# Optimization experiments

Hardware: AMD Instinct MI355X
Metric: run time of the kernel (lower is better)

The kernel has to match this reference:

```python
import jax, jax.numpy as jnp
import numpy as np

DIM = 128
NUM_HEADS = 4
WH, WW = 7, 7
N = WH * WW            # 49 tokens per window
NW = 64                # number of windows (56/7)^2
BATCH = 64
B_ = BATCH * NW        # 4096


def _relative_position_index(Wh, Ww):
    coords = np.stack(np.meshgrid(np.arange(Wh), np.arange(Ww), indexing='ij'))  # [2,Wh,Ww]
    coords = coords.reshape(2, -1)
    rel = coords[:, :, None] - coords[:, None, :]          # [2, N, N]
    rel = rel.transpose(1, 2, 0).astype(np.int64)          # [N, N, 2]
    rel[:, :, 0] += Wh - 1
    rel[:, :, 1] += Ww - 1
    rel[:, :, 0] *= 2 * Ww - 1
    return rel.sum(-1)                                     # [N, N]


def setup_inputs() -> dict:
    key = jax.random.key(0)
    ks = jax.random.split(key, 8)
    x = jax.random.normal(ks[0], (B_, N, DIM), dtype=jnp.float32)
    # Swin shift-mask: additive, 0 or large negative; random floats are fine for math check
    mask = jax.random.normal(ks[1], (NW, N, N), dtype=jnp.float32)
    qkv_w = jax.random.normal(ks[2], (DIM, 3 * DIM), dtype=jnp.float32) * 0.02
    qkv_b = jax.random.normal(ks[3], (3 * DIM,), dtype=jnp.float32) * 0.02
    proj_w = jax.random.normal(ks[4], (DIM, DIM), dtype=jnp.float32) * 0.02
    proj_b = jax.random.normal(ks[5], (DIM,), dtype=jnp.float32) * 0.02
    table_size = (2 * WH - 1) * (2 * WW - 1)  # 169
    bias_table = jax.random.normal(ks[6], (table_size, NUM_HEADS), dtype=jnp.float32) * 0.02
    rel_idx = jnp.asarray(_relative_position_index(WH, WW), dtype=jnp.int32)  # [N,N]
    return {"x": x, "mask": mask, "qkv_w": qkv_w, "qkv_b": qkv_b,
            "proj_w": proj_w, "proj_b": proj_b, "bias_table": bias_table,
            "rel_idx": rel_idx}


def reference(x, mask, qkv_w, qkv_b, proj_w, proj_b, bias_table, rel_idx):
    B, Nn, C = x.shape
    H = bias_table.shape[1]
    hd = C // H
    scale = hd ** -0.5
    # qkv projection -> [3, B, H, N, hd]
    qkv = (x @ qkv_w + qkv_b).reshape(B, Nn, 3, H, hd).transpose(2, 0, 3, 1, 4)
    q, k, v = qkv[0] * scale, qkv[1], qkv[2]
    attn = jnp.einsum('bhnd,bhmd->bhnm', q, k)  # [B,H,N,N]
    # gathered relative position bias -> [H,N,N]
    bias = bias_table[rel_idx.reshape(-1)].reshape(Nn, Nn, H).transpose(2, 0, 1)
    attn = attn + bias[None]
    nW = mask.shape[0]
    attn = attn.reshape(-1, nW, H, Nn, Nn) + mask[None, :, None].astype(attn.dtype)
    attn = jax.nn.softmax(attn.reshape(-1, H, Nn, Nn), axis=-1)
    out = jnp.einsum('bhnm,bhmd->bnhd', attn, v).reshape(B, Nn, C)
    return out @ proj_w + proj_b
```

## Files before the change

### kernel.cpp

```cpp
#include <hip/hip_runtime.h>

#define NTOK 49
#define DIMC 128
#define NH   4
#define NWIN 64
#define NBLK 4096

#define WPROJ_OFF 98304
#define BMF_OFF   131072

typedef unsigned short u16x8 __attribute__((ext_vector_type(8)));
typedef __bf16        bf16x8 __attribute__((ext_vector_type(8)));
typedef float         f32x4  __attribute__((ext_vector_type(4)));

__device__ __forceinline__ unsigned short f2bf(float f) {
  return __builtin_bit_cast(unsigned short, (__bf16)f);
}

__device__ __forceinline__ bf16x8 ld_frag(const unsigned short* p) {
  return __builtin_bit_cast(bf16x8, *(const u16x8*)p);
}

__device__ __forceinline__ bf16x8 pack_bf16x8(float4 lo, float4 hi) {
  bf16x8 r;
  r[0] = (__bf16)lo.x; r[1] = (__bf16)lo.y; r[2] = (__bf16)lo.z; r[3] = (__bf16)lo.w;
  r[4] = (__bf16)hi.x; r[5] = (__bf16)hi.y; r[6] = (__bf16)hi.z; r[7] = (__bf16)hi.w;
  return r;
}

#define MFMA(a, b, c) __builtin_amdgcn_mfma_f32_16x16x32_bf16(a, b, c, 0, 0, 0)

__global__ void prep_kernel(const float* __restrict__ qkv_w,
                            const float* __restrict__ proj_w,
                            const float* __restrict__ bias_table,
                            const int*   __restrict__ rel_idx,
                            const float* __restrict__ mask,
                            unsigned short* __restrict__ wqkv,
                            unsigned short* __restrict__ wproj,
                            float* __restrict__ bmf)
{
  const int tid = blockIdx.x * blockDim.x + threadIdx.x;
  const int nth = gridDim.x * blockDim.x;

  for (int idx = tid; idx < 4*24*64*8; idx += nth) {
    int ii = idx & 7, lane = (idx >> 3) & 63, rest = idx >> 9;
    int ct = rest % 24, kt = rest / 24;
    int k = kt*32 + ((lane >> 4) << 3) + ii;
    int c = ct*16 + (lane & 15);
    wqkv[idx] = f2bf(qkv_w[k*384 + c]);
  }
  for (int idx = tid; idx < 4*8*64*8; idx += nth) {
    int ii = idx & 7, lane = (idx >> 3) & 63, rest = idx >> 9;
    int ct = rest & 7, kt = rest >> 3;
    int k = kt*32 + ((lane >> 4) << 3) + ii;
    int c = ct*16 + (lane & 15);
    wproj[idx] = f2bf(proj_w[k*128 + c]);
  }
  for (int idx = tid; idx < NWIN*NH*16*256; idx += nth) {
    int r2   = idx & 3;
    int lane = (idx >> 2) & 63;
    int ij   = (idx >> 8) & 15;
    int h    = (idx >> 12) & 3;
    int wi   = idx >> 14;
    int i = ij >> 2, j = ij & 3;
    int r = i*16 + ((lane >> 4) << 2) + r2;
    int c = j*16 + (lane & 15);
    float v = -1e30f;
    if (r < NTOK && c < NTOK)
      v = mask[wi*2401 + r*49 + c] + bias_table[rel_idx[r*49 + c]*4 + h];
    bmf[idx] = v;
  }
}

#define SLOT 5712
__global__ __launch_bounds__(256, 3) void winattn_kernel(
    const float* __restrict__ x,
    const float* __restrict__ qkv_b,
    const float* __restrict__ proj_b,
    const unsigned short* __restrict__ wqkv,
    const unsigned short* __restrict__ wproj,
    const float* __restrict__ bmf,
    float* __restrict__ out)
{
  __shared__ __align__(16) unsigned short smem[4*SLOT];

  const int b    = blockIdx.x;
  const int wi   = b & (NWIN - 1);
  const int tid  = threadIdx.x;
  const int h    = tid >> 6;
  const int lane = tid & 63;
  const int lhi  = lane >> 4;
  const int llo  = lane & 15;

  unsigned short* slot = smem + h*SLOT;
  unsigned short* Qh  = slot;
  unsigned short* Kh  = slot + 1764;
  unsigned short* Vh  = slot + 3528;
  unsigned short* Ph  = slot;
  unsigned short* XOh = slot;

  const f32x4 zv = {0.f, 0.f, 0.f, 0.f};
  const float* xb = x + (size_t)b * (NTOK*DIMC);

  f32x4 acc[6][4];
  #pragma unroll
  for (int j = 0; j < 6; j++)
    #pragma unroll
    for (int i = 0; i < 4; i++) acc[j][i] = zv;

  #pragma unroll
  for (int kt = 0; kt < 4; kt++) {
    bf16x8 a[4];
    #pragma unroll
    for (int i = 0; i < 4; i++) {
      float4 lo = make_float4(0.f,0.f,0.f,0.f), hi = lo;
      int row = i*16 + llo;
      if (i < 3 || row < NTOK) {
        const float4* p = (const float4*)(xb + row*DIMC + kt*32 + lhi*8);
        lo = p[0]; hi = p[1];
      }
      a[i] = pack_bf16x8(lo, hi);
    }
    #pragma unroll
    for (int j = 0; j < 6; j++) {
      int ct = (j >> 1)*8 + h*2 + (j & 1);
      bf16x8 bw = ld_frag(wqkv + (((kt*24 + ct)*64 + lane) << 3));
      #pragma unroll
      for (int i = 0; i < 4; i++) acc[j][i] = MFMA(a[i], bw, acc[j][i]);
    }
  }

  float bias[6];
  #pragma unroll
  for (int j = 0; j < 6; j++)
    bias[j] = qkv_b[((j >> 1)*8 + h*2 + (j & 1))*16 + llo];

  const float scale = 0.17677669529663687f;

  #pragma unroll
  for (int j = 0; j < 2; j++) {
    int d = j*16 + llo;
    #pragma unroll
    for (int i = 0; i < 4; i++)
      #pragma unroll
      for (int r2 = 0; r2 < 4; r2++) {
        int r = i*16 + lhi*4 + r2;
        if (r < NTOK) Qh[r*36 + d] = f2bf((acc[j][i][r2] + bias[j]) * scale);
      }
  }
  #pragma unroll
  for (int j = 2; j < 4; j++) {
    int d = (j - 2)*16 + llo;
    #pragma unroll
    for (int i = 0; i < 4; i++)
      #pragma unroll
      for (int r2 = 0; r2 < 4; r2++) {
        int r = i*16 + lhi*4 + r2;
        if (r < NTOK) Kh[r*36 + d] = f2bf(acc[j][i][r2] + bias[j]);
      }
  }
  #pragma unroll
  for (int j = 4; j < 6; j++) {
    int d = (j - 4)*16 + llo;
    #pragma unroll
    for (int i = 0; i < 4; i++) {
      ushort4 pk;
      pk.x = f2bf(acc[j][i][0] + bias[j]);
      pk.y = f2bf(acc[j][i][1] + bias[j]);
      pk.z = f2bf(acc[j][i][2] + bias[j]);
      pk.w = f2bf(acc[j][i][3] + bias[j]);
      *(ushort4*)(Vh + d*68 + i*16 + lhi*4) = pk;
    }
  }

  f32x4 s[4][4];
  #pragma unroll
  for (int i = 0; i < 4; i++)
    #pragma unroll
    for (int j = 0; j < 4; j++) s[i][j] = zv;

  {
    bf16x8 qa[4];
    #pragma unroll
    for (int i = 0; i < 4; i++) qa[i] = ld_frag(Qh + (i*16 + llo)*36 + lhi*8);
    #pragma unroll
    for (int j = 0; j < 4; j++) {
      bf16x8 kb = ld_frag(Kh + (j*16 + llo)*36 + lhi*8);
      #pragma unroll
      for (int i = 0; i < 4; i++) s[i][j] = MFMA(qa[i], kb, s[i][j]);
    }
  }

  {
    const float4* bmf4 = (const float4*)bmf + (size_t)(wi*4 + h)*16*64 + lane;
    #pragma unroll
    for (int j = 0; j < 4; j++) {
      bool cok = (j*16 + llo) < NTOK;
      #pragma unroll
      for (int i = 0; i < 4; i++) {
        float4 t = bmf4[(i*4 + j)*64];
        #pragma unroll
        for (int r2 = 0; r2 < 4; r2++) {
          float v = s[i][j][r2] + (&t.x)[r2];
          s[i][j][r2] = cok ? v : -1e30f;
        }
      }
    }
  }

  #pragma unroll
  for (int i = 0; i < 4; i++) {
    #pragma unroll
    for (int r2 = 0; r2 < 4; r2++) {
      float m = fmaxf(fmaxf(s[i][0][r2], s[i][1][r2]),
                      fmaxf(s[i][2][r2], s[i][3][r2]));
      #pragma unroll
      for (int off = 1; off < 16; off <<= 1) m = fmaxf(m, __shfl_xor(m, off, 64));
      float sum = 0.f;
      #pragma unroll
      for (int j = 0; j < 4; j++) {
        float p = __expf(s[i][j][r2] - m);
        s[i][j][r2] = p;
        sum += p;
      }
      #pragma unroll
      for (int off = 1; off < 16; off <<= 1) sum += __shfl_xor(sum, off, 64);
      float inv = 1.0f / sum;
      #pragma unroll
      for (int j = 0; j < 4; j++) s[i][j][r2] *= inv;
    }
  }

  #pragma unroll
  for (int i = 0; i < 4; i++)
    #pragma unroll
    for (int r2 = 0; r2 < 4; r2++) {
      int r = i*16 + lhi*4 + r2;
      if (r < NTOK) {
        #pragma unroll
        for (int j = 0; j < 4; j++)
          Ph[r*72 + j*16 + llo] = f2bf(s[i][j][r2]);
      }
    }

  f32x4 oacc[2][4];
  #pragma unroll
  for (int nt = 0; nt < 2; nt++)
    #pragma unroll
    for (int i = 0; i < 4; i++) oacc[nt][i] = zv;

  #pragma unroll
  for (int ks = 0; ks < 2; ks++) {
    bf16x8 pa[4];
    #pragma unroll
    for (int i = 0; i < 4; i++)
      pa[i] = ld_frag(Ph + (i*16 + llo)*72 + ks*32 + lhi*8);
    #pragma unroll
    for (int nt = 0; nt < 2; nt++) {
      bf16x8 vb = ld_frag(Vh + (nt*16 + llo)*68 + ks*32 + lhi*8);
      #pragma unroll
      for (int i = 0; i < 4; i++) oacc[nt][i] = MFMA(pa[i], vb, oacc[nt][i]);
    }
  }

  #pragma unroll
  for (int nt = 0; nt < 2; nt++)
    #pragma unroll
    for (int i = 0; i < 4; i++)
      #pragma unroll
      for (int r2 = 0; r2 < 4; r2++) {
        int r = i*16 + lhi*4 + r2;
        if (r < NTOK) XOh[r*36 + nt*16 + llo] = f2bf(oacc[nt][i][r2]);
      }

  __syncthreads();

  {
    f32x4 pacc[2][4];
    #pragma unroll
    for (int j = 0; j < 2; j++)
      #pragma unroll
      for (int i = 0; i < 4; i++) pacc[j][i] = zv;

    #pragma unroll
    for (int kt = 0; kt < 4; kt++) {
      bf16x8 a[4];
      #pragma unroll
      for (int i = 0; i < 4; i++)
        a[i] = ld_frag(smem + kt*SLOT + (i*16 + llo)*36 + lhi*8);
      #pragma unroll
      for (int j = 0; j < 2; j++) {
        int ct = h*2 + j;
        bf16x8 bw = ld_frag(wproj + (((kt*8 + ct)*64 + lane) << 3));
        #pragma unroll
        for (int i = 0; i < 4; i++) pacc[j][i] = MFMA(a[i], bw, pacc[j][i]);
      }
    }

    float* op = out + (size_t)b * (NTOK*DIMC);
    #pragma unroll
    for (int j = 0; j < 2; j++) {
      int c = (h*2 + j)*16 + llo;
      float pb = proj_b[c];
      #pragma unroll
      for (int i = 0; i < 4; i++)
        #pragma unroll
        for (int r2 = 0; r2 < 4; r2++) {
          int r = i*16 + lhi*4 + r2;
          if (r < NTOK) op[r*128 + c] = pacc[j][i][r2] + pb;
        }
    }
  }
}

extern "C" void kernel_launch(void* const* d_in, const int* in_sizes, int n_in,
                              void* d_out, int out_size, void* d_ws, size_t ws_size,
                              hipStream_t stream)
{
  const float* x          = (const float*)d_in[0];
  const float* mask       = (const float*)d_in[1];
  const float* qkv_w      = (const float*)d_in[2];
  const float* qkv_b      = (const float*)d_in[3];
  const float* proj_w     = (const float*)d_in[4];
  const float* proj_b     = (const float*)d_in[5];
  const float* bias_table = (const float*)d_in[6];
  const int*   rel_idx    = (const int*)d_in[7];
  float* out = (float*)d_out;

  unsigned short* wqkv  = (unsigned short*)d_ws;
  unsigned short* wproj = (unsigned short*)((char*)d_ws + WPROJ_OFF);
  float*          bmf   = (float*)((char*)d_ws + BMF_OFF);

  prep_kernel<<<1024, 256, 0, stream>>>(qkv_w, proj_w, bias_table, rel_idx, mask,
                                        wqkv, wproj, bmf);
  winattn_kernel<<<NBLK, 256, 0, stream>>>(x, qkv_b, proj_b, wqkv, wproj, bmf, out);
}
```

Before: 129.7 us.

## Drop softmax max pass and compute row sums via ones-column MFMA

```diff
diff --git a/kernel.cpp b/kernel.cpp
--- a/kernel.cpp
+++ b/kernel.cpp
@@ -72,7 +72,7 @@
   }
 }
 
-#define SLOT 5712
+#define SLOT 5772
 __global__ __launch_bounds__(256, 3) void winattn_kernel(
     const float* __restrict__ x,
     const float* __restrict__ qkv_b,
@@ -82,7 +82,7 @@
     const float* __restrict__ bmf,
     float* __restrict__ out)
 {
-  __shared__ __align__(16) unsigned short smem[4*SLOT];
+  __shared__ __align__(16) unsigned short smem[24112];
 
   const int b    = blockIdx.x;
   const int wi   = b & (NWIN - 1);
@@ -148,6 +148,14 @@
         if (r < NTOK) Qh[r*36 + d] = f2bf((acc[j][i][r2] + bias[j]) * scale);
       }
   }
+
+  float4 bmv[16];
+  {
+    const float4* bmf4 = (const float4*)bmf + (size_t)(wi*4 + h)*16*64 + lane;
+    #pragma unroll
+    for (int t = 0; t < 16; t++) bmv[t] = bmf4[t*64];
+  }
+
   #pragma unroll
   for (int j = 2; j < 4; j++) {
     int d = (j - 2)*16 + llo;
@@ -172,6 +180,7 @@
       *(ushort4*)(Vh + d*68 + i*16 + lhi*4) = pk;
     }
   }
+  Vh[32*68 + lane] = 0x3F80;
 
   f32x4 s[4][4];
   #pragma unroll
@@ -191,43 +200,17 @@
     }
   }
 
-  {
-    const float4* bmf4 = (const float4*)bmf + (size_t)(wi*4 + h)*16*64 + lane;
-    #pragma unroll
-    for (int j = 0; j < 4; j++) {
-      bool cok = (j*16 + llo) < NTOK;
-      #pragma unroll
-      for (int i = 0; i < 4; i++) {
-        float4 t = bmf4[(i*4 + j)*64];
-        #pragma unroll
-        for (int r2 = 0; r2 < 4; r2++) {
-          float v = s[i][j][r2] + (&t.x)[r2];
-          s[i][j][r2] = cok ? v : -1e30f;
-        }
-      }
-    }
-  }
-
-  #pragma unroll
-  for (int i = 0; i < 4; i++) {
-    #pragma unroll
-    for (int r2 = 0; r2 < 4; r2++) {
-      float m = fmaxf(fmaxf(s[i][0][r2], s[i][1][r2]),
-                      fmaxf(s[i][2][r2], s[i][3][r2]));
-      #pragma unroll
-      for (int off = 1; off < 16; off <<= 1) m = fmaxf(m, __shfl_xor(m, off, 64));
-      float sum = 0.f;
-      #pragma unroll
-      for (int j = 0; j < 4; j++) {
-        float p = __expf(s[i][j][r2] - m);
-        s[i][j][r2] = p;
-        sum += p;
-      }
-      #pragma unroll
-      for (int off = 1; off < 16; off <<= 1) sum += __shfl_xor(sum, off, 64);
-      float inv = 1.0f / sum;
-      #pragma unroll
-      for (int j = 0; j < 4; j++) s[i][j][r2] *= inv;
+  #pragma unroll
+  for (int j = 0; j < 4; j++) {
+    bool cok = (j*16 + llo) < NTOK;
+    #pragma unroll
+    for (int i = 0; i < 4; i++) {
+      float4 t = bmv[i*4 + j];
+      #pragma unroll
+      for (int r2 = 0; r2 < 4; r2++) {
+        float v = s[i][j][r2] + (&t.x)[r2];
+        s[i][j][r2] = __expf(cok ? v : -1e30f);
+      }
     }
   }
 
@@ -243,11 +226,9 @@
       }
     }
 
-  f32x4 oacc[2][4];
-  #pragma unroll
-  for (int nt = 0; nt < 2; nt++)
-    #pragma unroll
-    for (int i = 0; i < 4; i++) oacc[nt][i] = zv;
+  f32x4 oacc[2][4], osum[4];
+  #pragma unroll
+  for (int i = 0; i < 4; i++) { oacc[0][i] = zv; oacc[1][i] = zv; osum[i] = zv; }
 
   #pragma unroll
   for (int ks = 0; ks < 2; ks++) {
@@ -256,12 +237,25 @@
     for (int i = 0; i < 4; i++)
       pa[i] = ld_frag(Ph + (i*16 + llo)*72 + ks*32 + lhi*8);
     #pragma unroll
-    for (int nt = 0; nt < 2; nt++) {
+    for (int nt = 0; nt < 3; nt++) {
       bf16x8 vb = ld_frag(Vh + (nt*16 + llo)*68 + ks*32 + lhi*8);
       #pragma unroll
-      for (int i = 0; i < 4; i++) oacc[nt][i] = MFMA(pa[i], vb, oacc[nt][i]);
-    }
-  }
+      for (int i = 0; i < 4; i++) {
+        if (nt < 2) oacc[nt][i] = MFMA(pa[i], vb, oacc[nt][i]);
+        else        osum[i]     = MFMA(pa[i], vb, osum[i]);
+      }
+    }
+  }
+
+  #pragma unroll
+  for (int i = 0; i < 4; i++)
+    #pragma unroll
+    for (int r2 = 0; r2 < 4; r2++) {
+      float sm  = __shfl(osum[i][r2], lane & 48, 64);
+      float inv = __builtin_amdgcn_rcpf(sm);
+      oacc[0][i][r2] *= inv;
+      oacc[1][i][r2] *= inv;
+    }
 
   #pragma unroll
   for (int nt = 0; nt < 2; nt++)
```

Result: no change. 127.8 us (-1.4%).
